# Optimization experiments

Measured on AMD Instinct MI355X. Metric: run time of the kernel, lower is better.

The kernel has to match this reference:

```python
import jax, jax.numpy as jnp
import numpy as np

B, T, D, H = 8, 4096, 1024, 1024

def setup_inputs() -> dict:
    key = jax.random.key(0)
    k1, k2, k3, k4, k5 = jax.random.split(key, 5)
    s = 1.0 / np.sqrt(D)  # nn.Linear default init scale
    return {
        "x": jax.random.normal(k1, (B, T, D), dtype=jnp.float32),
        "Wz": jax.random.uniform(k2, (H, D), dtype=jnp.float32, minval=-s, maxval=s),
        "bz": jax.random.uniform(k3, (H,), dtype=jnp.float32, minval=-s, maxval=s),
        "Wh": jax.random.uniform(k4, (H, D), dtype=jnp.float32, minval=-s, maxval=s),
        "bh": jax.random.uniform(k5, (H,), dtype=jnp.float32, minval=-s, maxval=s),
    }

def log_g(x):
    # Appendix B.3 of 'Were RNNs All We Needed?'
    return jnp.where(x >= 0, jnp.log(jax.nn.relu(x) + 0.5), -jax.nn.softplus(-x))

def reference(x, Wz, bz, Wh, bh):
    # Linear projections: [B,T,D] @ [D,H] -> [B,T,H]
    k = jnp.einsum('btd,hd->bth', x, Wz) + bz
    tilde_h = jnp.einsum('btd,hd->bth', x, Wh) + bh
    log_z = -jax.nn.softplus(-k)           # log sigmoid(k)
    log_one_minus_z = -jax.nn.softplus(k)  # log (1 - sigmoid(k))
    log_tilde_h = log_g(tilde_h)
    # parallel scan in log space: h[i] = a[i]*h[i-1] + b[i]
    log_a_star = jnp.cumsum(log_one_minus_z, axis=1)
    log_x = log_a_star + jax.lax.cumlogsumexp(log_z + log_tilde_h - log_a_star, axis=1)
    return jnp.exp(log_x)
```

## Files before the change

### kernel.cpp

```cpp
#include <hip/hip_runtime.h>
#include <cstdint>

typedef unsigned short u16;
typedef __attribute__((ext_vector_type(8))) __bf16 bf16x8_t;
typedef __attribute__((ext_vector_type(4))) float f32x4_t;
typedef __attribute__((ext_vector_type(4))) uint32_t u32x4_t;

constexpr int Bn = 8, Tn = 4096, Dn = 1024, Hn = 1024;
constexpr int Mn = Bn * Tn;
constexpr int NC = 128, CL = Tn / NC;

__device__ __forceinline__ u16 f2bf(float f) {
  uint32_t u = __builtin_bit_cast(uint32_t, f);
  u += 0x7FFFu + ((u >> 16) & 1u);
  return (u16)(u >> 16);
}

__global__ __launch_bounds__(256) void cvt_all(
    const float* __restrict__ x, const float* __restrict__ wz, const float* __restrict__ wh,
    u16* __restrict__ xb, u16* __restrict__ wzb, u16* __restrict__ whb) {
  int i = blockIdx.x * 256 + threadIdx.x;
  const float* s; u16* d; int off;
  if (i < 8388608)      { s = x;  d = xb;  off = i; }
  else if (i < 8650752) { s = wz; d = wzb; off = i - 8388608; }
  else                  { s = wh; d = whb; off = i - 8650752; }
  f32x4_t v = __builtin_nontemporal_load(&((const f32x4_t*)s)[off]);
  ushort4 o;
  o.x = f2bf(v.x); o.y = f2bf(v.y); o.z = f2bf(v.z); o.w = f2bf(v.w);
  ((ushort4*)d)[off] = o;
}

__device__ __forceinline__ void gl_lds16(const void* g, void* l) {
  __builtin_amdgcn_global_load_lds((const __attribute__((address_space(1))) void*)g,
                                   (__attribute__((address_space(3))) void*)l, 16u, 0, 0u);
}

__device__ __forceinline__ void gates(float kv, float tv, float& a, float& bb) {
  float e  = __expf(-kv);
  float rc = __builtin_amdgcn_rcpf(1.f + e);
  a = e * rc;
  float g = (tv >= 0.f) ? (tv + 0.5f)
                        : __builtin_amdgcn_rcpf(1.f + __expf(-tv));
  bb = rc * g;
}

__global__ __launch_bounds__(256) void gemm_fused(
    const u16* __restrict__ A, const u16* __restrict__ Wz, const u16* __restrict__ Wh,
    const float* __restrict__ bz, const float* __restrict__ bh,
    uint32_t* __restrict__ gAB, float* __restrict__ Aagg, float* __restrict__ Bagg) {
  constexpr int K = 1024;
  const uint bid = blockIdx.x;
  const uint xcd = bid & 7;
  const uint seq = bid >> 3;
  const uint ht  = seq & 15;
  const uint mt  = (seq >> 4) * 8 + xcd;
  const int m0 = mt * 128;
  const int h0 = ht * 64;

  __shared__ u16 lA[128 * 32];
  __shared__ u16 lB[2][64 * 32];

  const int tid  = threadIdx.x;
  const int lane = tid & 63;
  const int wave = tid >> 6;

  const int csA = (((lane & 3) ^ ((lane >> 3) & 3)) * 8);
  const int csB = (((tid  & 3) ^ ((tid  >> 3) & 3)) * 8);
  const u16* gA0 = A  + (size_t)(m0 + wave * 16 + (lane >> 2)) * K + csA;
  const u16* gBz = Wz + (size_t)(h0 + (tid >> 2)) * K + csB;
  const u16* gBh = Wh + (size_t)(h0 + (tid >> 2)) * K + csB;
  u16* lAw  = lA    + wave * 512;
  u16* lBw0 = lB[0] + wave * 512;
  u16* lBw1 = lB[1] + wave * 512;

  const int fr   = lane & 15;
  const int KB   = lane >> 4;
  const int fcol = (KB ^ ((fr >> 1) & 3)) * 8;

  f32x4_t az[2][4] = {}, ah[2][4] = {};

  for (int kt = 0; kt < K; kt += 32) {
    gl_lds16(gA0 + kt,                    lAw);
    gl_lds16(gA0 + kt + (size_t)64 * K,   lAw + 2048);
    gl_lds16(gBz + kt,                    lBw0);
    gl_lds16(gBh + kt,                    lBw1);
    __syncthreads();
    bf16x8_t af[2], bzf[4], bhf[4];
#pragma unroll
    for (int i = 0; i < 2; ++i)
      af[i] = *(const bf16x8_t*)&lA[(wave * 32 + i * 16 + fr) * 32 + fcol];
#pragma unroll
    for (int j = 0; j < 4; ++j) {
      bzf[j] = *(const bf16x8_t*)&lB[0][(j * 16 + fr) * 32 + fcol];
      bhf[j] = *(const bf16x8_t*)&lB[1][(j * 16 + fr) * 32 + fcol];
    }
#pragma unroll
    for (int i = 0; i < 2; ++i)
#pragma unroll
      for (int j = 0; j < 4; ++j) {
        az[i][j] = __builtin_amdgcn_mfma_f32_16x16x32_bf16(af[i], bzf[j], az[i][j], 0, 0, 0);
        ah[i][j] = __builtin_amdgcn_mfma_f32_16x16x32_bf16(af[i], bhf[j], ah[i][j], 0, 0, 0);
      }
    __syncthreads();
  }

  const int cr = (lane >> 4) * 4;
  const int cc = lane & 15;
  const int b  = mt >> 5;
  const int tc = (mt & 31) * 4 + wave;

#pragma unroll
  for (int j = 0; j < 4; ++j) {
    float bvz = bz[h0 + j * 16 + cc];
    float bvh = bh[h0 + j * 16 + cc];
    float Ai[2], Bi[2];
#pragma unroll
    for (int i = 0; i < 2; ++i) {
      float Al = 1.f, Bl = 0.f;
#pragma unroll
      for (int r = 0; r < 4; ++r) {
        float kv = az[i][j][r] + bvz;
        float tv = ah[i][j][r] + bvh;
        float a, bb;
        gates(kv, tv, a, bb);
        _Float16 a16 = (_Float16)a, b16 = (_Float16)bb;
        uint32_t pk = (uint32_t)__builtin_bit_cast(u16, a16) |
                      ((uint32_t)__builtin_bit_cast(u16, b16) << 16);
        __builtin_nontemporal_store(
            pk, &gAB[(size_t)(m0 + wave * 32 + i * 16 + cr + r) * Hn + h0 + j * 16 + cc]);
        float ar = (float)a16, br = (float)b16;
        Al = Al * ar;
        Bl = fmaf(ar, Bl, br);
      }
      float Ahi = __shfl_down(Al, 16), Bhi = __shfl_down(Bl, 16);
      float A2 = Ahi * Al;
      float B2 = fmaf(Ahi, Bl, Bhi);
      Ahi = __shfl_down(A2, 32); Bhi = __shfl_down(B2, 32);
      Ai[i] = Ahi * A2;
      Bi[i] = fmaf(Ahi, B2, Bhi);
    }
    float Aw = Ai[1] * Ai[0];
    float Bw = fmaf(Ai[1], Bi[0], Bi[1]);
    if (lane < 16) {
      size_t ai = ((size_t)(b * NC + tc)) * Hn + h0 + j * 16 + lane;
      Aagg[ai] = Aw;
      Bagg[ai] = Bw;
    }
  }
}

__global__ __launch_bounds__(64) void scan_phase_b(
    const float* Aagg, const float* __restrict__ Bagg, float* carry) {
  int h = blockIdx.x * 64 + threadIdx.x;
  int b = blockIdx.y;
  const size_t base = (size_t)b * NC * Hn + h;
  float state = 0.f;
  constexpr int PF = 16;
  float Av[PF], Bv[PF];
  for (int g = 0; g < NC; g += PF) {
#pragma unroll
    for (int u = 0; u < PF; ++u) {
      size_t idx = base + (size_t)(g + u) * Hn;
      Av[u] = Aagg[idx];
      Bv[u] = Bagg[idx];
    }
#pragma unroll
    for (int u = 0; u < PF; ++u) {
      size_t idx = base + (size_t)(g + u) * Hn;
      carry[idx] = state;
      state = fmaf(Av[u], state, Bv[u]);
    }
  }
}

__global__ __launch_bounds__(256) void scan_phase_c(
    const uint32_t* __restrict__ gAB, const float* __restrict__ carry,
    float* __restrict__ out) {
  int h0 = threadIdx.x * 4;
  int c = blockIdx.x, b = blockIdx.y;
  f32x4_t hst = *(const f32x4_t*)(carry + ((size_t)(b * NC + c)) * Hn + h0);
  size_t base = ((size_t)b * Tn + (size_t)c * CL) * Hn + h0;
#pragma unroll 4
  for (int t = 0; t < CL; ++t) {
    size_t idx = base + (size_t)t * Hn;
    u32x4_t v = __builtin_nontemporal_load((const u32x4_t*)(gAB + idx));
    uint32_t vv[4] = {v.x, v.y, v.z, v.w};
#pragma unroll
    for (int u = 0; u < 4; ++u) {
      float a = (float)__builtin_bit_cast(_Float16, (u16)(vv[u] & 0xFFFFu));
      float bb = (float)__builtin_bit_cast(_Float16, (u16)(vv[u] >> 16));
      hst[u] = fmaf(a, hst[u], bb);
    }
    __builtin_nontemporal_store(hst, (f32x4_t*)(out + idx));
  }
}

extern "C" void kernel_launch(void* const* d_in, const int* in_sizes, int n_in,
                              void* d_out, int out_size, void* d_ws, size_t ws_size,
                              hipStream_t stream) {
  const float* x  = (const float*)d_in[0];
  const float* Wz = (const float*)d_in[1];
  const float* bz = (const float*)d_in[2];
  const float* Wh = (const float*)d_in[3];
  const float* bh = (const float*)d_in[4];
  float* out = (float*)d_out;

  char* ws = (char*)d_ws;
  u16*      xbf   = (u16*)     (ws);
  u16*      wzbf  = (u16*)     (ws + 67108864);
  u16*      whbf  = (u16*)     (ws + 69206016);
  uint32_t* gAB   = (uint32_t*)(ws + 71303168);
  float*    Aagg  = (float*)   (ws + 205520896);
  float*    Bagg  = (float*)   (ws + 209715200);
  float*    carry = Aagg;

  cvt_all<<<dim3(34816), 256, 0, stream>>>(x, Wz, Wh, xbf, wzbf, whbf);
  gemm_fused<<<dim3(4096), 256, 0, stream>>>(xbf, wzbf, whbf, bz, bh, gAB, Aagg, Bagg);
  scan_phase_b<<<dim3(16, Bn), 64, 0, stream>>>(Aagg, Bagg, carry);
  scan_phase_c<<<dim3(NC, Bn), 256, 0, stream>>>(gAB, carry, out);
}
```

Baseline: 443.8 us.

## Fuse scan into GEMM epilogue with decoupled look-back across tiles

Merges the chunk scan phases into the GEMM kernel. Each block takes a dynamic tile id from an atomic counter and scans its tile in registers and LDS. It then waits on a flag from the previous time-tile in the same chain to get the incoming carry, publishes its own prefix, and writes the final output directly. This removes the fp16 gate buffer round trip to HBM and two extra kernel launches. In exchange it adds a serial chain of 32 tiles per (batch, h-tile) with spin-waiting, and a bounded spin that could silently yield wrong results on timeout.

```diff
diff --git a/kernel.cpp b/kernel.cpp
--- a/kernel.cpp
+++ b/kernel.cpp
@@ -4,11 +4,9 @@
 typedef unsigned short u16;
 typedef __attribute__((ext_vector_type(8))) __bf16 bf16x8_t;
 typedef __attribute__((ext_vector_type(4))) float f32x4_t;
-typedef __attribute__((ext_vector_type(4))) uint32_t u32x4_t;
 
 constexpr int Bn = 8, Tn = 4096, Dn = 1024, Hn = 1024;
 constexpr int Mn = Bn * Tn;
-constexpr int NC = 128, CL = Tn / NC;
 
 __device__ __forceinline__ u16 f2bf(float f) {
   uint32_t u = __builtin_bit_cast(uint32_t, f);
@@ -18,8 +16,13 @@
 
 __global__ __launch_bounds__(256) void cvt_all(
     const float* __restrict__ x, const float* __restrict__ wz, const float* __restrict__ wh,
-    u16* __restrict__ xb, u16* __restrict__ wzb, u16* __restrict__ whb) {
+    u16* __restrict__ xb, u16* __restrict__ wzb, u16* __restrict__ whb,
+    uint32_t* __restrict__ vcounter, uint32_t* __restrict__ flags) {
   int i = blockIdx.x * 256 + threadIdx.x;
+  if (i < 4097) {
+    if (i == 0) *vcounter = 0u;
+    else        flags[i - 1] = 0u;
+  }
   const float* s; u16* d; int off;
   if (i < 8388608)      { s = x;  d = xb;  off = i; }
   else if (i < 8650752) { s = wz; d = wzb; off = i - 8388608; }
@@ -44,21 +47,31 @@
   bb = rc * g;
 }
 
-__global__ __launch_bounds__(256) void gemm_fused(
+__global__ __launch_bounds__(256) void gemm_scan(
     const u16* __restrict__ A, const u16* __restrict__ Wz, const u16* __restrict__ Wh,
     const float* __restrict__ bz, const float* __restrict__ bh,
-    uint32_t* __restrict__ gAB, float* __restrict__ Aagg, float* __restrict__ Bagg) {
+    float* __restrict__ out,
+    uint32_t* __restrict__ vcounter, uint32_t* __restrict__ flags,
+    float* __restrict__ prefA, float* __restrict__ prefB) {
   constexpr int K = 1024;
-  const uint bid = blockIdx.x;
+
+  __shared__ uint vidS;
+  if (threadIdx.x == 0)
+    vidS = __hip_atomic_fetch_add(vcounter, 1u, __ATOMIC_RELAXED, __HIP_MEMORY_SCOPE_AGENT);
+
+  __shared__ u16 lA[128 * 32];
+  __shared__ u16 lB[2][64 * 32];
+  __shared__ float aggL[4][64][2];
+  __shared__ float carryL[64];
+
+  __syncthreads();
+  const uint bid = vidS;
   const uint xcd = bid & 7;
   const uint seq = bid >> 3;
   const uint ht  = seq & 15;
   const uint mt  = (seq >> 4) * 8 + xcd;
   const int m0 = mt * 128;
   const int h0 = ht * 64;
-
-  __shared__ u16 lA[128 * 32];
-  __shared__ u16 lB[2][64 * 32];
 
   const int tid  = threadIdx.x;
   const int lane = tid & 63;
@@ -104,19 +117,23 @@
     __syncthreads();
   }
 
-  const int cr = (lane >> 4) * 4;
   const int cc = lane & 15;
+  const int q  = lane >> 4;
   const int b  = mt >> 5;
-  const int tc = (mt & 31) * 4 + wave;
+  const int p  = mt & 31;
+  const int chain = b * 16 + (int)ht;
+
+  uint32_t pk[4][2][4];
+  float EA[4][2], EB[4][2];
 
 #pragma unroll
   for (int j = 0; j < 4; ++j) {
     float bvz = bz[h0 + j * 16 + cc];
     float bvh = bh[h0 + j * 16 + cc];
-    float Ai[2], Bi[2];
+    float FA0 = 1.f, FB0 = 0.f;
 #pragma unroll
     for (int i = 0; i < 2; ++i) {
-      float Al = 1.f, Bl = 0.f;
+      float A4 = 1.f, B4 = 0.f;
 #pragma unroll
       for (int r = 0; r < 4; ++r) {
         float kv = az[i][j][r] + bvz;
@@ -124,74 +141,95 @@
         float a, bb;
         gates(kv, tv, a, bb);
         _Float16 a16 = (_Float16)a, b16 = (_Float16)bb;
-        uint32_t pk = (uint32_t)__builtin_bit_cast(u16, a16) |
+        pk[j][i][r] = (uint32_t)__builtin_bit_cast(u16, a16) |
                       ((uint32_t)__builtin_bit_cast(u16, b16) << 16);
+        float ar = (float)a16, br = (float)b16;
+        B4 = fmaf(ar, B4, br);
+        A4 = A4 * ar;
+      }
+      float IA = A4, IB = B4;
+      float tA = __shfl_up(IA, 16), tB = __shfl_up(IB, 16);
+      if (q >= 1) { IB = fmaf(IA, tB, IB); IA *= tA; }
+      tA = __shfl_up(IA, 32); tB = __shfl_up(IB, 32);
+      if (q >= 2) { IB = fmaf(IA, tB, IB); IA *= tA; }
+      float eA = __shfl_up(IA, 16), eB = __shfl_up(IB, 16);
+      if (q == 0) { eA = 1.f; eB = 0.f; }
+      if (i == 0) {
+        EA[j][0] = eA; EB[j][0] = eB;
+        FA0 = __shfl(IA, 48 + cc);
+        FB0 = __shfl(IB, 48 + cc);
+      } else {
+        EA[j][1] = eA * FA0;
+        EB[j][1] = fmaf(eA, FB0, eB);
+        if (q == 3) {
+          aggL[wave][j * 16 + cc][0] = IA * FA0;
+          aggL[wave][j * 16 + cc][1] = fmaf(IA, FB0, IB);
+        }
+      }
+    }
+  }
+  __syncthreads();
+
+  if (wave == 0) {
+    const int col = lane;
+    float bA = aggL[0][col][0], bB = aggL[0][col][1];
+#pragma unroll
+    for (int w = 1; w < 4; ++w) {
+      float cA = aggL[w][col][0], cB = aggL[w][col][1];
+      bB = fmaf(cA, bB, cB);
+      bA = cA * bA;
+    }
+    float vA = bA, vB = bB;
+    float v0 = 0.f;
+    if (p > 0) {
+      const uint32_t* fp = flags + chain * 32 + (p - 1);
+      int spins = 0;
+      while (__hip_atomic_load(fp, __ATOMIC_ACQUIRE, __HIP_MEMORY_SCOPE_AGENT) == 0u) {
+        __builtin_amdgcn_s_sleep(8);
+        if (++spins > (1 << 20)) break;
+      }
+      size_t pb = ((size_t)chain * 32 + (p - 1)) * 64 + col;
+      uint32_t ua = __hip_atomic_load((const uint32_t*)(prefA + pb),
+                                      __ATOMIC_RELAXED, __HIP_MEMORY_SCOPE_AGENT);
+      uint32_t ub = __hip_atomic_load((const uint32_t*)(prefB + pb),
+                                      __ATOMIC_RELAXED, __HIP_MEMORY_SCOPE_AGENT);
+      float pA = __builtin_bit_cast(float, ua);
+      float pB = __builtin_bit_cast(float, ub);
+      v0 = pB;
+      vB = fmaf(bA, pB, bB);
+      vA = bA * pA;
+    }
+    size_t ob = ((size_t)chain * 32 + p) * 64 + col;
+    __hip_atomic_store((uint32_t*)(prefA + ob), __builtin_bit_cast(uint32_t, vA),
+                       __ATOMIC_RELAXED, __HIP_MEMORY_SCOPE_AGENT);
+    __hip_atomic_store((uint32_t*)(prefB + ob), __builtin_bit_cast(uint32_t, vB),
+                       __ATOMIC_RELAXED, __HIP_MEMORY_SCOPE_AGENT);
+    if (lane == 0)
+      __hip_atomic_store(flags + chain * 32 + p, 1u,
+                         __ATOMIC_RELEASE, __HIP_MEMORY_SCOPE_AGENT);
+    carryL[col] = v0;
+  }
+  __syncthreads();
+
+#pragma unroll
+  for (int j = 0; j < 4; ++j) {
+    const int col = j * 16 + cc;
+    float v = carryL[col];
+    for (int w = 0; w < wave; ++w)
+      v = fmaf(aggL[w][col][0], v, aggL[w][col][1]);
+#pragma unroll
+    for (int i = 0; i < 2; ++i) {
+      float h = fmaf(EA[j][i], v, EB[j][i]);
+#pragma unroll
+      for (int r = 0; r < 4; ++r) {
+        uint32_t w32 = pk[j][i][r];
+        float a  = (float)__builtin_bit_cast(_Float16, (u16)(w32 & 0xFFFFu));
+        float bb = (float)__builtin_bit_cast(_Float16, (u16)(w32 >> 16));
+        h = fmaf(a, h, bb);
         __builtin_nontemporal_store(
-            pk, &gAB[(size_t)(m0 + wave * 32 + i * 16 + cr + r) * Hn + h0 + j * 16 + cc]);
-        float ar = (float)a16, br = (float)b16;
-        Al = Al * ar;
-        Bl = fmaf(ar, Bl, br);
-      }
-      float Ahi = __shfl_down(Al, 16), Bhi = __shfl_down(Bl, 16);
-      float A2 = Ahi * Al;
-      float B2 = fmaf(Ahi, Bl, Bhi);
-      Ahi = __shfl_down(A2, 32); Bhi = __shfl_down(B2, 32);
-      Ai[i] = Ahi * A2;
-      Bi[i] = fmaf(Ahi, B2, Bhi);
-    }
-    float Aw = Ai[1] * Ai[0];
-    float Bw = fmaf(Ai[1], Bi[0], Bi[1]);
-    if (lane < 16) {
-      size_t ai = ((size_t)(b * NC + tc)) * Hn + h0 + j * 16 + lane;
-      Aagg[ai] = Aw;
-      Bagg[ai] = Bw;
-    }
-  }
-}
-
-__global__ __launch_bounds__(64) void scan_phase_b(
-    const float* Aagg, const float* __restrict__ Bagg, float* carry) {
-  int h = blockIdx.x * 64 + threadIdx.x;
-  int b = blockIdx.y;
-  const size_t base = (size_t)b * NC * Hn + h;
-  float state = 0.f;
-  constexpr int PF = 16;
-  float Av[PF], Bv[PF];
-  for (int g = 0; g < NC; g += PF) {
-#pragma unroll
-    for (int u = 0; u < PF; ++u) {
-      size_t idx = base + (size_t)(g + u) * Hn;
-      Av[u] = Aagg[idx];
-      Bv[u] = Bagg[idx];
-    }
-#pragma unroll
-    for (int u = 0; u < PF; ++u) {
-      size_t idx = base + (size_t)(g + u) * Hn;
-      carry[idx] = state;
-      state = fmaf(Av[u], state, Bv[u]);
-    }
-  }
-}
-
-__global__ __launch_bounds__(256) void scan_phase_c(
-    const uint32_t* __restrict__ gAB, const float* __restrict__ carry,
-    float* __restrict__ out) {
-  int h0 = threadIdx.x * 4;
-  int c = blockIdx.x, b = blockIdx.y;
-  f32x4_t hst = *(const f32x4_t*)(carry + ((size_t)(b * NC + c)) * Hn + h0);
-  size_t base = ((size_t)b * Tn + (size_t)c * CL) * Hn + h0;
-#pragma unroll 4
-  for (int t = 0; t < CL; ++t) {
-    size_t idx = base + (size_t)t * Hn;
-    u32x4_t v = __builtin_nontemporal_load((const u32x4_t*)(gAB + idx));
-    uint32_t vv[4] = {v.x, v.y, v.z, v.w};
-#pragma unroll
-    for (int u = 0; u < 4; ++u) {
-      float a = (float)__builtin_bit_cast(_Float16, (u16)(vv[u] & 0xFFFFu));
-      float bb = (float)__builtin_bit_cast(_Float16, (u16)(vv[u] >> 16));
-      hst[u] = fmaf(a, hst[u], bb);
-    }
-    __builtin_nontemporal_store(hst, (f32x4_t*)(out + idx));
+            h, &out[(size_t)(m0 + wave * 32 + i * 16 + q * 4 + r) * Hn + h0 + col]);
+      }
+    }
   }
 }
 
@@ -209,13 +247,12 @@
   u16*      xbf   = (u16*)     (ws);
   u16*      wzbf  = (u16*)     (ws + 67108864);
   u16*      whbf  = (u16*)     (ws + 69206016);
-  uint32_t* gAB   = (uint32_t*)(ws + 71303168);
-  float*    Aagg  = (float*)   (ws + 205520896);
-  float*    Bagg  = (float*)   (ws + 209715200);
-  float*    carry = Aagg;
-
-  cvt_all<<<dim3(34816), 256, 0, stream>>>(x, Wz, Wh, xbf, wzbf, whbf);
-  gemm_fused<<<dim3(4096), 256, 0, stream>>>(xbf, wzbf, whbf, bz, bh, gAB, Aagg, Bagg);
-  scan_phase_b<<<dim3(16, Bn), 64, 0, stream>>>(Aagg, Bagg, carry);
-  scan_phase_c<<<dim3(NC, Bn), 256, 0, stream>>>(gAB, carry, out);
-}
+  uint32_t* vcnt  = (uint32_t*)(ws + 71303168);
+  uint32_t* flags = (uint32_t*)(ws + 71303424);
+  float*    prefA = (float*)   (ws + 71319808);
+  float*    prefB = (float*)   (ws + 72368384);
+
+  cvt_all<<<dim3(34816), 256, 0, stream>>>(x, Wz, Wh, xbf, wzbf, whbf, vcnt, flags);
+  gemm_scan<<<dim3(4096), 256, 0, stream>>>(xbf, wzbf, whbf, bz, bh, out,
+                                            vcnt, flags, prefA, prefB);
+}
```

After: 1.315 ms. 196% more time.

## Use 2x2 wave tiling and K=64 per barrier in fused gate GEMM

Applied to the files above, without the earlier changes.

Changes the wave layout of the fused GEMM from four waves each owning 32 rows by all 64 columns to a 2x2 grid where each wave owns 64 rows by 32 columns. This raises fragment reuse per LDS read. Each iteration now stages two 32-wide K slices, halving the number of barrier round trips. The epilogue is reindexed so chunk aggregates still map to 32-row chunks. LDS usage doubles and register pressure for the A fragments rises.

```diff
diff --git a/kernel.cpp b/kernel.cpp
--- a/kernel.cpp
+++ b/kernel.cpp
@@ -57,94 +57,107 @@
   const int m0 = mt * 128;
   const int h0 = ht * 64;
 
-  __shared__ u16 lA[128 * 32];
-  __shared__ u16 lB[2][64 * 32];
+  __shared__ u16 lA [2][128 * 32];
+  __shared__ u16 lBz[2][64 * 32];
+  __shared__ u16 lBh[2][64 * 32];
 
   const int tid  = threadIdx.x;
   const int lane = tid & 63;
   const int wave = tid >> 6;
+  const int wm   = wave >> 1;
+  const int wh   = wave & 1;
 
   const int csA = (((lane & 3) ^ ((lane >> 3) & 3)) * 8);
   const int csB = (((tid  & 3) ^ ((tid  >> 3) & 3)) * 8);
   const u16* gA0 = A  + (size_t)(m0 + wave * 16 + (lane >> 2)) * K + csA;
   const u16* gBz = Wz + (size_t)(h0 + (tid >> 2)) * K + csB;
   const u16* gBh = Wh + (size_t)(h0 + (tid >> 2)) * K + csB;
-  u16* lAw  = lA    + wave * 512;
-  u16* lBw0 = lB[0] + wave * 512;
-  u16* lBw1 = lB[1] + wave * 512;
+  const int woff = wave * 512;
 
   const int fr   = lane & 15;
   const int KB   = lane >> 4;
   const int fcol = (KB ^ ((fr >> 1) & 3)) * 8;
 
-  f32x4_t az[2][4] = {}, ah[2][4] = {};
-
-  for (int kt = 0; kt < K; kt += 32) {
-    gl_lds16(gA0 + kt,                    lAw);
-    gl_lds16(gA0 + kt + (size_t)64 * K,   lAw + 2048);
-    gl_lds16(gBz + kt,                    lBw0);
-    gl_lds16(gBh + kt,                    lBw1);
+  f32x4_t az[4][2] = {}, ah[4][2] = {};
+
+  for (int kt = 0; kt < K; kt += 64) {
+    gl_lds16(gA0 + kt,                         lA[0] + woff);
+    gl_lds16(gA0 + kt + (size_t)64 * K,        lA[0] + woff + 2048);
+    gl_lds16(gA0 + kt + 32,                    lA[1] + woff);
+    gl_lds16(gA0 + kt + 32 + (size_t)64 * K,   lA[1] + woff + 2048);
+    gl_lds16(gBz + kt,                         lBz[0] + woff);
+    gl_lds16(gBz + kt + 32,                    lBz[1] + woff);
+    gl_lds16(gBh + kt,                         lBh[0] + woff);
+    gl_lds16(gBh + kt + 32,                    lBh[1] + woff);
     __syncthreads();
-    bf16x8_t af[2], bzf[4], bhf[4];
-#pragma unroll
-    for (int i = 0; i < 2; ++i)
-      af[i] = *(const bf16x8_t*)&lA[(wave * 32 + i * 16 + fr) * 32 + fcol];
-#pragma unroll
-    for (int j = 0; j < 4; ++j) {
-      bzf[j] = *(const bf16x8_t*)&lB[0][(j * 16 + fr) * 32 + fcol];
-      bhf[j] = *(const bf16x8_t*)&lB[1][(j * 16 + fr) * 32 + fcol];
-    }
-#pragma unroll
-    for (int i = 0; i < 2; ++i)
-#pragma unroll
-      for (int j = 0; j < 4; ++j) {
-        az[i][j] = __builtin_amdgcn_mfma_f32_16x16x32_bf16(af[i], bzf[j], az[i][j], 0, 0, 0);
-        ah[i][j] = __builtin_amdgcn_mfma_f32_16x16x32_bf16(af[i], bhf[j], ah[i][j], 0, 0, 0);
+#pragma unroll
+    for (int half = 0; half < 2; ++half) {
+      bf16x8_t af[4], bzf[2], bhf[2];
+#pragma unroll
+      for (int i = 0; i < 4; ++i)
+        af[i] = *(const bf16x8_t*)&lA[half][(wm * 64 + i * 16 + fr) * 32 + fcol];
+#pragma unroll
+      for (int j = 0; j < 2; ++j) {
+        bzf[j] = *(const bf16x8_t*)&lBz[half][(wh * 32 + j * 16 + fr) * 32 + fcol];
+        bhf[j] = *(const bf16x8_t*)&lBh[half][(wh * 32 + j * 16 + fr) * 32 + fcol];
       }
+#pragma unroll
+      for (int i = 0; i < 4; ++i)
+#pragma unroll
+        for (int j = 0; j < 2; ++j) {
+          az[i][j] = __builtin_amdgcn_mfma_f32_16x16x32_bf16(af[i], bzf[j], az[i][j], 0, 0, 0);
+          ah[i][j] = __builtin_amdgcn_mfma_f32_16x16x32_bf16(af[i], bhf[j], ah[i][j], 0, 0, 0);
+        }
+    }
     __syncthreads();
   }
 
   const int cr = (lane >> 4) * 4;
   const int cc = lane & 15;
   const int b  = mt >> 5;
-  const int tc = (mt & 31) * 4 + wave;
-
-#pragma unroll
-  for (int j = 0; j < 4; ++j) {
-    float bvz = bz[h0 + j * 16 + cc];
-    float bvh = bh[h0 + j * 16 + cc];
-    float Ai[2], Bi[2];
-#pragma unroll
-    for (int i = 0; i < 2; ++i) {
-      float Al = 1.f, Bl = 0.f;
-#pragma unroll
-      for (int r = 0; r < 4; ++r) {
-        float kv = az[i][j][r] + bvz;
-        float tv = ah[i][j][r] + bvh;
-        float a, bb;
-        gates(kv, tv, a, bb);
-        _Float16 a16 = (_Float16)a, b16 = (_Float16)bb;
-        uint32_t pk = (uint32_t)__builtin_bit_cast(u16, a16) |
-                      ((uint32_t)__builtin_bit_cast(u16, b16) << 16);
-        __builtin_nontemporal_store(
-            pk, &gAB[(size_t)(m0 + wave * 32 + i * 16 + cr + r) * Hn + h0 + j * 16 + cc]);
-        float ar = (float)a16, br = (float)b16;
-        Al = Al * ar;
-        Bl = fmaf(ar, Bl, br);
+
+#pragma unroll
+  for (int j = 0; j < 2; ++j) {
+    float bvz = bz[h0 + wh * 32 + j * 16 + cc];
+    float bvh = bh[h0 + wh * 32 + j * 16 + cc];
+#pragma unroll
+    for (int cp = 0; cp < 2; ++cp) {
+      float Ai[2], Bi[2];
+#pragma unroll
+      for (int i2 = 0; i2 < 2; ++i2) {
+        const int i = cp * 2 + i2;
+        float Al = 1.f, Bl = 0.f;
+#pragma unroll
+        for (int r = 0; r < 4; ++r) {
+          float kv = az[i][j][r] + bvz;
+          float tv = ah[i][j][r] + bvh;
+          float a, bb;
+          gates(kv, tv, a, bb);
+          _Float16 a16 = (_Float16)a, b16 = (_Float16)bb;
+          uint32_t pk = (uint32_t)__builtin_bit_cast(u16, a16) |
+                        ((uint32_t)__builtin_bit_cast(u16, b16) << 16);
+          __builtin_nontemporal_store(
+              pk, &gAB[(size_t)(m0 + wm * 64 + i * 16 + cr + r) * Hn +
+                       h0 + wh * 32 + j * 16 + cc]);
+          float ar = (float)a16, br = (float)b16;
+          Al = Al * ar;
+          Bl = fmaf(ar, Bl, br);
+        }
+        float Ahi = __shfl_down(Al, 16), Bhi = __shfl_down(Bl, 16);
+        float A2 = Ahi * Al;
+        float B2 = fmaf(Ahi, Bl, Bhi);
+        Ahi = __shfl_down(A2, 32); Bhi = __shfl_down(B2, 32);
+        Ai[i2] = Ahi * A2;
+        Bi[i2] = fmaf(Ahi, B2, Bhi);
       }
-      float Ahi = __shfl_down(Al, 16), Bhi = __shfl_down(Bl, 16);
-      float A2 = Ahi * Al;
-      float B2 = fmaf(Ahi, Bl, Bhi);
-      Ahi = __shfl_down(A2, 32); Bhi = __shfl_down(B2, 32);
-      Ai[i] = Ahi * A2;
-      Bi[i] = fmaf(Ahi, B2, Bhi);
-    }
-    float Aw = Ai[1] * Ai[0];
-    float Bw = fmaf(Ai[1], Bi[0], Bi[1]);
-    if (lane < 16) {
-      size_t ai = ((size_t)(b * NC + tc)) * Hn + h0 + j * 16 + lane;
-      Aagg[ai] = Aw;
-      Bagg[ai] = Bw;
+      float Aw = Ai[1] * Ai[0];
+      float Bw = fmaf(Ai[1], Bi[0], Bi[1]);
+      if (lane < 16) {
+        const int tc = (mt & 31) * 4 + wm * 2 + cp;
+        size_t ai = ((size_t)(b * NC + tc)) * Hn + h0 + wh * 32 + j * 16 + lane;
+        Aagg[ai] = Aw;
+        Bagg[ai] = Bw;
+      }
     }
   }
 }
```

Result: no change. 439.8 us (-0.9%).
